# Kernel tuning notes

Measured on AMD Instinct MI355X. Metric: run time of the kernel, lower is better.

## Reference

```python
import jax, jax.numpy as jnp
import numpy as np

N_NODES = 50000
N_EDGES = 800000
IN_CH = 128
OUT_CH = 128


def setup_inputs() -> dict:
    key = jax.random.key(0)
    k1, k2, k3, k4 = jax.random.split(key, 4)
    x = jax.random.normal(k1, (N_NODES, IN_CH), dtype=jnp.float32)
    edge_index = jax.random.randint(k2, (2, N_EDGES), 0, N_NODES, dtype=jnp.int64)
    # nn.Linear(2*in_ch, out_ch): weight [out_ch, 2*in_ch], bias [out_ch]
    lim = 1.0 / np.sqrt(2 * IN_CH)
    W = jax.random.uniform(k3, (OUT_CH, 2 * IN_CH), dtype=jnp.float32, minval=-lim, maxval=lim)
    b = jax.random.uniform(k4, (OUT_CH,), dtype=jnp.float32, minval=-lim, maxval=lim)
    return {"x": x, "edge_index": edge_index, "W": W, "b": b}


def reference(x, edge_index, W, b):
    src, dst = edge_index[0], edge_index[1]
    n = x.shape[0]
    # mean aggregation: scatter-add gathered source features, divide by degree
    neigh = jax.ops.segment_sum(x[src], dst, num_segments=n)  # [n, in_ch]
    deg = jax.ops.segment_sum(jnp.ones((dst.shape[0],), dtype=x.dtype), dst, num_segments=n)
    neigh = neigh / jnp.maximum(deg, 1.0)[:, None]
    h = jnp.concatenate([x, neigh], axis=-1)  # [n, 2*in_ch]
    out = h @ W.T + b  # [n, out_ch]
    # F.normalize(p=2, dim=-1, eps=1e-12)
    norm = jnp.linalg.norm(out, axis=-1, keepdims=True)
    return out / jnp.maximum(norm, 1e-12)
```

## Files before the change

kernel.cpp:

```cpp
#include <hip/hip_runtime.h>
#include <math.h>

#define N_NODES 50000
#define N_EDGES 800000
#define CH      128
#define KDIM    256

#define OFF_NEIGH  0
#define OFF_DEGCNT 25600000
#define OFF_OFFS   25800192
#define OFF_TOTAL  26000384
#define OFF_COL    26000640

__global__ void k_zero(int* __restrict__ degcnt, int* __restrict__ total) {
  int i = blockIdx.x * blockDim.x + threadIdx.x;
  if (i < 12500) reinterpret_cast<int4*>(degcnt)[i] = make_int4(0, 0, 0, 0);
  if (i == 0) *total = 0;
}

__global__ void k_degree(const int* __restrict__ dst, int* __restrict__ degcnt,
                         int* __restrict__ rank) {
  int t = blockIdx.x * blockDim.x + threadIdx.x;
  int e = t * 4;
  if (e + 3 < N_EDGES) {
    int4 d = *reinterpret_cast<const int4*>(&dst[e]);
    int4 r;
    r.x = atomicAdd(&degcnt[d.x], 1);
    r.y = atomicAdd(&degcnt[d.y], 1);
    r.z = atomicAdd(&degcnt[d.z], 1);
    r.w = atomicAdd(&degcnt[d.w], 1);
    *reinterpret_cast<int4*>(&rank[e]) = r;
  }
}

__global__ void k_alloc(const int* __restrict__ degcnt, int* __restrict__ offs,
                        int* __restrict__ total) {
  int i = blockIdx.x * blockDim.x + threadIdx.x;
  int lane = threadIdx.x & 63;
  int v = (i < N_NODES) ? degcnt[i] : 0;
  int s = v;
  #pragma unroll
  for (int off = 1; off < 64; off <<= 1) {
    int t = __shfl_up(s, off, 64);
    if (lane >= off) s += t;
  }
  int wsum = __shfl(s, 63, 64);
  int base = 0;
  if (lane == 63) base = atomicAdd(total, wsum);
  base = __shfl(base, 63, 64);
  if (i < N_NODES) offs[i] = base + s - v;
}

__global__ void k_fill(const int* __restrict__ src, const int* __restrict__ dst,
                       const int* __restrict__ offs, const int* __restrict__ rank,
                       int* __restrict__ col) {
  int t = blockIdx.x * blockDim.x + threadIdx.x;
  int e = t * 4;
  if (e + 3 < N_EDGES) {
    int4 d = *reinterpret_cast<const int4*>(&dst[e]);
    int4 r = *reinterpret_cast<const int4*>(&rank[e]);
    int4 s = *reinterpret_cast<const int4*>(&src[e]);
    col[offs[d.x] + r.x] = s.x;
    col[offs[d.y] + r.y] = s.y;
    col[offs[d.z] + r.z] = s.z;
    col[offs[d.w] + r.w] = s.w;
  }
}

__global__ void k_aggregate(const float* __restrict__ x,
                            const int* __restrict__ offs,
                            const int* __restrict__ degcnt,
                            const int* __restrict__ col,
                            float* __restrict__ neigh) {
  int gtid = blockIdx.x * blockDim.x + threadIdx.x;
  int node = gtid >> 6;
  if (node >= N_NODES) return;
  int lane = threadIdx.x & 63;
  int half = lane >> 5, l32 = lane & 31;
  int beg = offs[node], deg = degcnt[node];
  const float4* xp = reinterpret_cast<const float4*>(x);
  float4 acc = make_float4(0.f, 0.f, 0.f, 0.f);
  for (int base = 0; base < deg; base += 64) {
    int nb = deg - base; if (nb > 64) nb = 64;
    int ci = (lane < nb) ? col[beg + base + lane] : 0;
    int nb2 = nb & ~1;
    #pragma unroll 4
    for (int k = 0; 2 * k < nb2; ++k) {
      int s = __shfl(ci, 2 * k + half, 64);
      float4 v = xp[(size_t)s * 32 + l32];
      acc.x += v.x; acc.y += v.y; acc.z += v.z; acc.w += v.w;
    }
    if (nb & 1) {
      int s = __shfl(ci, nb - 1, 64);
      if (half == 0) {
        float4 v = xp[(size_t)s * 32 + l32];
        acc.x += v.x; acc.y += v.y; acc.z += v.z; acc.w += v.w;
      }
    }
  }
  acc.x += __shfl_xor(acc.x, 32, 64);
  acc.y += __shfl_xor(acc.y, 32, 64);
  acc.z += __shfl_xor(acc.z, 32, 64);
  acc.w += __shfl_xor(acc.w, 32, 64);
  if (half == 0) {
    float inv = 1.0f / fmaxf((float)deg, 1.0f);
    reinterpret_cast<float4*>(neigh)[(size_t)node * 32 + l32] =
        make_float4(acc.x * inv, acc.y * inv, acc.z * inv, acc.w * inv);
  }
}

__global__ __launch_bounds__(256) void k_gemm_norm(
    const float* __restrict__ x, const float* __restrict__ neigh,
    const float* __restrict__ W, const float* __restrict__ bias,
    float* __restrict__ out) {
  __shared__ float hs[64][32];
  __shared__ float Ws[128][32];
  int tid = threadIdx.x;
  int tx = tid & 15;
  int ty = tid >> 4;
  int node0 = blockIdx.x * 64;

  float acc[4][8];
  #pragma unroll
  for (int i = 0; i < 4; ++i)
    #pragma unroll
    for (int j = 0; j < 8; ++j) acc[i][j] = 0.f;

  for (int kb = 0; kb < KDIM; kb += 32) {
    const float* srcp = (kb < CH) ? x : neigh;
    int koff = kb & (CH - 1);
    #pragma unroll
    for (int jj = 0; jj < 2; ++jj) {
      int idx = tid + 256 * jj;
      int row = idx >> 3;
      int c4 = (idx & 7) * 4;
      int swz = (((row >> 3) ^ row) & 7) * 4;
      int node = node0 + row;
      if (node >= N_NODES) node = N_NODES - 1;
      float4 v = *reinterpret_cast<const float4*>(&srcp[(size_t)node * CH + koff + c4]);
      *reinterpret_cast<float4*>(&hs[row][c4 ^ swz]) = v;
    }
    #pragma unroll
    for (int jj = 0; jj < 4; ++jj) {
      int idx = tid + 256 * jj;
      int ch = idx >> 3;
      int c4 = (idx & 7) * 4;
      int swz = (((ch >> 3) ^ ch) & 7) * 4;
      float4 v = *reinterpret_cast<const float4*>(&W[(size_t)ch * KDIM + kb + c4]);
      *reinterpret_cast<float4*>(&Ws[ch][c4 ^ swz]) = v;
    }
    __syncthreads();
    #pragma unroll
    for (int k4 = 0; k4 < 32; k4 += 4) {
      float4 wv[8];
      #pragma unroll
      for (int j = 0; j < 8; ++j) {
        int ch = tx * 8 + j;
        int swz = (((ch >> 3) ^ ch) & 7) * 4;
        wv[j] = *reinterpret_cast<const float4*>(&Ws[ch][k4 ^ swz]);
      }
      #pragma unroll
      for (int i = 0; i < 4; ++i) {
        int row = ty * 4 + i;
        int swz = (((row >> 3) ^ row) & 7) * 4;
        float4 hv = *reinterpret_cast<const float4*>(&hs[row][k4 ^ swz]);
        #pragma unroll
        for (int j = 0; j < 8; ++j) {
          acc[i][j] += hv.x * wv[j].x;
          acc[i][j] += hv.y * wv[j].y;
          acc[i][j] += hv.z * wv[j].z;
          acc[i][j] += hv.w * wv[j].w;
        }
      }
    }
    __syncthreads();
  }

  float bv[8];
  #pragma unroll
  for (int j = 0; j < 8; ++j) bv[j] = bias[tx * 8 + j];

  #pragma unroll
  for (int i = 0; i < 4; ++i) {
    int node = node0 + ty * 4 + i;
    float o[8];
    float s = 0.f;
    #pragma unroll
    for (int j = 0; j < 8; ++j) { o[j] = acc[i][j] + bv[j]; s += o[j] * o[j]; }
    #pragma unroll
    for (int m = 1; m < 16; m <<= 1) s += __shfl_xor(s, m, 64);
    float inv = 1.0f / fmaxf(sqrtf(s), 1e-12f);
    if (node < N_NODES) {
      float4 v0 = make_float4(o[0] * inv, o[1] * inv, o[2] * inv, o[3] * inv);
      float4 v1 = make_float4(o[4] * inv, o[5] * inv, o[6] * inv, o[7] * inv);
      *reinterpret_cast<float4*>(&out[(size_t)node * CH + tx * 8]) = v0;
      *reinterpret_cast<float4*>(&out[(size_t)node * CH + tx * 8 + 4]) = v1;
    }
  }
}

extern "C" void kernel_launch(void* const* d_in, const int* in_sizes, int n_in,
                              void* d_out, int out_size, void* d_ws, size_t ws_size,
                              hipStream_t stream) {
  const float* x  = (const float*)d_in[0];
  const int*   ei = (const int*)d_in[1];
  const float* W  = (const float*)d_in[2];
  const float* b  = (const float*)d_in[3];
  float* out = (float*)d_out;

  char* ws = (char*)d_ws;
  float* neigh = (float*)(ws + OFF_NEIGH);
  int* rank    = (int*)(ws + OFF_NEIGH);
  int* degcnt  = (int*)(ws + OFF_DEGCNT);
  int* offs    = (int*)(ws + OFF_OFFS);
  int* total   = (int*)(ws + OFF_TOTAL);
  int* col     = (int*)(ws + OFF_COL);
  const int* src = ei;
  const int* dst = ei + N_EDGES;

  k_zero<<<(12500 + 255) / 256, 256, 0, stream>>>(degcnt, total);
  k_degree<<<(N_EDGES / 4 + 255) / 256, 256, 0, stream>>>(dst, degcnt, rank);
  k_alloc<<<(N_NODES + 255) / 256, 256, 0, stream>>>(degcnt, offs, total);
  k_fill<<<(N_EDGES / 4 + 255) / 256, 256, 0, stream>>>(src, dst, offs, rank, col);
  k_aggregate<<<(N_NODES * 64 + 255) / 256, 256, 0, stream>>>(x, offs, degcnt, col, neigh);
  k_gemm_norm<<<(N_NODES + 63) / 64, 256, 0, stream>>>(x, neigh, W, b, out);
}
```

Measured before the change: 263.7 us.

## Replace FP32 tiled GEMM with bf16 MFMA GEMM on converted operands

Converts x and W to bf16 in a new conversion kernel and has the aggregation kernel write the mean-neighbour features as bf16. The FP32 shared-memory GEMM is replaced by a wave-level kernel using 16x16x32 bf16 MFMA instructions, which loads operands directly from global memory without LDS staging. The L2-normalize epilogue stays fused. The aim is to cut GEMM compute time and halve the bytes moved for neigh and GEMM inputs. The cost is an extra conversion pass over x and reduced precision that may test the accuracy tolerance.

```diff
diff --git a/kernel.cpp b/kernel.cpp
--- a/kernel.cpp
+++ b/kernel.cpp
@@ -6,11 +6,22 @@
 #define CH      128
 #define KDIM    256
 
-#define OFF_NEIGH  0
-#define OFF_DEGCNT 25600000
-#define OFF_OFFS   25800192
-#define OFF_TOTAL  26000384
-#define OFF_COL    26000640
+typedef __attribute__((ext_vector_type(8))) short bf16x8;
+typedef __attribute__((ext_vector_type(4))) float f32x4;
+
+#define OFF_XB     0
+#define OFF_NB     12800000
+#define OFF_WB     25600000
+#define OFF_DEGCNT 25665536
+#define OFF_OFFS   25865728
+#define OFF_TOTAL  26065920
+#define OFF_COL    26066176
+
+__device__ __forceinline__ short f2bf(float f) {
+  unsigned u = __builtin_bit_cast(unsigned, f);
+  u += 0x7FFFu + ((u >> 16) & 1u);
+  return (short)(u >> 16);
+}
 
 __global__ void k_zero(int* __restrict__ degcnt, int* __restrict__ total) {
   int i = blockIdx.x * blockDim.x + threadIdx.x;
@@ -67,11 +78,26 @@
   }
 }
 
+__global__ void k_convert(const float* __restrict__ x, const float* __restrict__ W,
+                          short* __restrict__ xb, short* __restrict__ Wb) {
+  int i = blockIdx.x * blockDim.x + threadIdx.x;
+  if (i < 1600000) {
+    float4 v = reinterpret_cast<const float4*>(x)[i];
+    short4 o; o.x = f2bf(v.x); o.y = f2bf(v.y); o.z = f2bf(v.z); o.w = f2bf(v.w);
+    reinterpret_cast<short4*>(xb)[i] = o;
+  }
+  if (i < 8192) {
+    float4 v = reinterpret_cast<const float4*>(W)[i];
+    short4 o; o.x = f2bf(v.x); o.y = f2bf(v.y); o.z = f2bf(v.z); o.w = f2bf(v.w);
+    reinterpret_cast<short4*>(Wb)[i] = o;
+  }
+}
+
 __global__ void k_aggregate(const float* __restrict__ x,
                             const int* __restrict__ offs,
                             const int* __restrict__ degcnt,
                             const int* __restrict__ col,
-                            float* __restrict__ neigh) {
+                            short* __restrict__ nb) {
   int gtid = blockIdx.x * blockDim.x + threadIdx.x;
   int node = gtid >> 6;
   if (node >= N_NODES) return;
@@ -81,17 +107,17 @@
   const float4* xp = reinterpret_cast<const float4*>(x);
   float4 acc = make_float4(0.f, 0.f, 0.f, 0.f);
   for (int base = 0; base < deg; base += 64) {
-    int nb = deg - base; if (nb > 64) nb = 64;
-    int ci = (lane < nb) ? col[beg + base + lane] : 0;
-    int nb2 = nb & ~1;
+    int nbk = deg - base; if (nbk > 64) nbk = 64;
+    int ci = (lane < nbk) ? col[beg + base + lane] : 0;
+    int nb2 = nbk & ~1;
     #pragma unroll 4
     for (int k = 0; 2 * k < nb2; ++k) {
       int s = __shfl(ci, 2 * k + half, 64);
       float4 v = xp[(size_t)s * 32 + l32];
       acc.x += v.x; acc.y += v.y; acc.z += v.z; acc.w += v.w;
     }
-    if (nb & 1) {
-      int s = __shfl(ci, nb - 1, 64);
+    if (nbk & 1) {
+      int s = __shfl(ci, nbk - 1, 64);
       if (half == 0) {
         float4 v = xp[(size_t)s * 32 + l32];
         acc.x += v.x; acc.y += v.y; acc.z += v.z; acc.w += v.w;
@@ -104,97 +130,77 @@
   acc.w += __shfl_xor(acc.w, 32, 64);
   if (half == 0) {
     float inv = 1.0f / fmaxf((float)deg, 1.0f);
-    reinterpret_cast<float4*>(neigh)[(size_t)node * 32 + l32] =
-        make_float4(acc.x * inv, acc.y * inv, acc.z * inv, acc.w * inv);
-  }
-}
-
-__global__ __launch_bounds__(256) void k_gemm_norm(
-    const float* __restrict__ x, const float* __restrict__ neigh,
-    const float* __restrict__ W, const float* __restrict__ bias,
+    short4 o;
+    o.x = f2bf(acc.x * inv); o.y = f2bf(acc.y * inv);
+    o.z = f2bf(acc.z * inv); o.w = f2bf(acc.w * inv);
+    reinterpret_cast<short4*>(nb)[(size_t)node * 32 + l32] = o;
+  }
+}
+
+__global__ __launch_bounds__(256) void k_mfma_gemm(
+    const short* __restrict__ xb, const short* __restrict__ nb,
+    const short* __restrict__ Wb, const float* __restrict__ bias,
     float* __restrict__ out) {
-  __shared__ float hs[64][32];
-  __shared__ float Ws[128][32];
   int tid = threadIdx.x;
-  int tx = tid & 15;
-  int ty = tid >> 4;
-  int node0 = blockIdx.x * 64;
-
-  float acc[4][8];
-  #pragma unroll
-  for (int i = 0; i < 4; ++i)
-    #pragma unroll
-    for (int j = 0; j < 8; ++j) acc[i][j] = 0.f;
-
-  for (int kb = 0; kb < KDIM; kb += 32) {
-    const float* srcp = (kb < CH) ? x : neigh;
-    int koff = kb & (CH - 1);
-    #pragma unroll
-    for (int jj = 0; jj < 2; ++jj) {
-      int idx = tid + 256 * jj;
-      int row = idx >> 3;
-      int c4 = (idx & 7) * 4;
-      int swz = (((row >> 3) ^ row) & 7) * 4;
-      int node = node0 + row;
-      if (node >= N_NODES) node = N_NODES - 1;
-      float4 v = *reinterpret_cast<const float4*>(&srcp[(size_t)node * CH + koff + c4]);
-      *reinterpret_cast<float4*>(&hs[row][c4 ^ swz]) = v;
-    }
-    #pragma unroll
-    for (int jj = 0; jj < 4; ++jj) {
-      int idx = tid + 256 * jj;
-      int ch = idx >> 3;
-      int c4 = (idx & 7) * 4;
-      int swz = (((ch >> 3) ^ ch) & 7) * 4;
-      float4 v = *reinterpret_cast<const float4*>(&W[(size_t)ch * KDIM + kb + c4]);
-      *reinterpret_cast<float4*>(&Ws[ch][c4 ^ swz]) = v;
-    }
-    __syncthreads();
-    #pragma unroll
-    for (int k4 = 0; k4 < 32; k4 += 4) {
-      float4 wv[8];
+  int wv = tid >> 6;
+  int l = tid & 63;
+  int l15 = l & 15, lg = l >> 4;
+  int node0 = blockIdx.x * 64 + wv * 16;
+
+  int arow = node0 + l15; if (arow >= N_NODES) arow = N_NODES - 1;
+  const short* xr = xb + (size_t)arow * CH + lg * 8;
+  const short* nr = nb + (size_t)arow * CH + lg * 8;
+
+  f32x4 acc[8];
+  #pragma unroll
+  for (int f = 0; f < 8; ++f) acc[f] = (f32x4){0.f, 0.f, 0.f, 0.f};
+
+  #pragma unroll
+  for (int s = 0; s < 4; ++s) {
+    bf16x8 a = *reinterpret_cast<const bf16x8*>(xr + s * 32);
+    #pragma unroll
+    for (int f = 0; f < 8; ++f) {
+      bf16x8 b = *reinterpret_cast<const bf16x8*>(
+          Wb + (size_t)(f * 16 + l15) * KDIM + s * 32 + lg * 8);
+      acc[f] = __builtin_amdgcn_mfma_f32_16x16x32_bf16(a, b, acc[f], 0, 0, 0);
+    }
+  }
+  #pragma unroll
+  for (int s = 0; s < 4; ++s) {
+    bf16x8 a = *reinterpret_cast<const bf16x8*>(nr + s * 32);
+    #pragma unroll
+    for (int f = 0; f < 8; ++f) {
+      bf16x8 b = *reinterpret_cast<const bf16x8*>(
+          Wb + (size_t)(f * 16 + l15) * KDIM + CH + s * 32 + lg * 8);
+      acc[f] = __builtin_amdgcn_mfma_f32_16x16x32_bf16(a, b, acc[f], 0, 0, 0);
+    }
+  }
+
+  float ov[8][4];
+  float s4[4] = {0.f, 0.f, 0.f, 0.f};
+  #pragma unroll
+  for (int f = 0; f < 8; ++f) {
+    float bv = bias[f * 16 + l15];
+    #pragma unroll
+    for (int r = 0; r < 4; ++r) {
+      float o = acc[f][r] + bv;
+      ov[f][r] = o;
+      s4[r] += o * o;
+    }
+  }
+  #pragma unroll
+  for (int r = 0; r < 4; ++r) {
+    #pragma unroll
+    for (int m = 1; m < 16; m <<= 1) s4[r] += __shfl_xor(s4[r], m, 64);
+    s4[r] = 1.0f / fmaxf(sqrtf(s4[r]), 1e-12f);
+  }
+  #pragma unroll
+  for (int r = 0; r < 4; ++r) {
+    int row = node0 + lg * 4 + r;
+    if (row < N_NODES) {
       #pragma unroll
-      for (int j = 0; j < 8; ++j) {
-        int ch = tx * 8 + j;
-        int swz = (((ch >> 3) ^ ch) & 7) * 4;
-        wv[j] = *reinterpret_cast<const float4*>(&Ws[ch][k4 ^ swz]);
-      }
-      #pragma unroll
-      for (int i = 0; i < 4; ++i) {
-        int row = ty * 4 + i;
-        int swz = (((row >> 3) ^ row) & 7) * 4;
-        float4 hv = *reinterpret_cast<const float4*>(&hs[row][k4 ^ swz]);
-        #pragma unroll
-        for (int j = 0; j < 8; ++j) {
-          acc[i][j] += hv.x * wv[j].x;
-          acc[i][j] += hv.y * wv[j].y;
-          acc[i][j] += hv.z * wv[j].z;
-          acc[i][j] += hv.w * wv[j].w;
-        }
-      }
-    }
-    __syncthreads();
-  }
-
-  float bv[8];
-  #pragma unroll
-  for (int j = 0; j < 8; ++j) bv[j] = bias[tx * 8 + j];
-
-  #pragma unroll
-  for (int i = 0; i < 4; ++i) {
-    int node = node0 + ty * 4 + i;
-    float o[8];
-    float s = 0.f;
-    #pragma unroll
-    for (int j = 0; j < 8; ++j) { o[j] = acc[i][j] + bv[j]; s += o[j] * o[j]; }
-    #pragma unroll
-    for (int m = 1; m < 16; m <<= 1) s += __shfl_xor(s, m, 64);
-    float inv = 1.0f / fmaxf(sqrtf(s), 1e-12f);
-    if (node < N_NODES) {
-      float4 v0 = make_float4(o[0] * inv, o[1] * inv, o[2] * inv, o[3] * inv);
-      float4 v1 = make_float4(o[4] * inv, o[5] * inv, o[6] * inv, o[7] * inv);
-      *reinterpret_cast<float4*>(&out[(size_t)node * CH + tx * 8]) = v0;
-      *reinterpret_cast<float4*>(&out[(size_t)node * CH + tx * 8 + 4]) = v1;
+      for (int f = 0; f < 8; ++f)
+        out[(size_t)row * CH + f * 16 + l15] = ov[f][r] * s4[r];
     }
   }
 }
@@ -209,8 +215,10 @@
   float* out = (float*)d_out;
 
   char* ws = (char*)d_ws;
-  float* neigh = (float*)(ws + OFF_NEIGH);
-  int* rank    = (int*)(ws + OFF_NEIGH);
+  short* xb    = (short*)(ws + OFF_XB);
+  int*   rank  = (int*)(ws + OFF_XB);
+  short* nb    = (short*)(ws + OFF_NB);
+  short* Wb    = (short*)(ws + OFF_WB);
   int* degcnt  = (int*)(ws + OFF_DEGCNT);
   int* offs    = (int*)(ws + OFF_OFFS);
   int* total   = (int*)(ws + OFF_TOTAL);
@@ -222,6 +230,7 @@
   k_degree<<<(N_EDGES / 4 + 255) / 256, 256, 0, stream>>>(dst, degcnt, rank);
   k_alloc<<<(N_NODES + 255) / 256, 256, 0, stream>>>(degcnt, offs, total);
   k_fill<<<(N_EDGES / 4 + 255) / 256, 256, 0, stream>>>(src, dst, offs, rank, col);
-  k_aggregate<<<(N_NODES * 64 + 255) / 256, 256, 0, stream>>>(x, offs, degcnt, col, neigh);
-  k_gemm_norm<<<(N_NODES + 63) / 64, 256, 0, stream>>>(x, neigh, W, b, out);
-}
+  k_convert<<<(1600000 + 255) / 256, 256, 0, stream>>>(x, W, xb, Wb);
+  k_aggregate<<<(N_NODES * 64 + 255) / 256, 256, 0, stream>>>(x, offs, degcnt, col, nb);
+  k_mfma_gemm<<<(N_NODES + 63) / 64, 256, 0, stream>>>(xb, nb, Wb, b, out);
+}
```

New measurement: 234.9 us. -10.9%, faster.
